# Optimization experiments

Measured on AMD Instinct MI355X. Metric: run time of the kernel, lower is better.

Reference implementation:

```python
import jax, jax.numpy as jnp
import numpy as np

MAX_ITER = 3  # matches init kwarg max_iter


def setup_inputs() -> dict:
    key = jax.random.key(0)
    k1, k2, k3, k4 = jax.random.split(key, 4)
    B, S = 4, 160
    return {
        "s_edge": jax.random.normal(k1, (B, S, S), dtype=jnp.float32),
        "s_sib": jax.random.normal(k2, (B, S, S, S), dtype=jnp.float32),
        "s_cop": jax.random.normal(k3, (B, S, S, S), dtype=jnp.float32),
        "s_grd": jax.random.normal(k4, (B, S, S, S), dtype=jnp.float32),
        "mask": jnp.ones((B, S, S), dtype=bool),
    }


def reference(s_edge, s_sib, s_cop, s_grd, mask):
    B, S, _ = mask.shape
    idx = jnp.arange(S)
    # Permute to the [head, mod, (sib), batch] layout used by the torch code.
    mask_p = jnp.transpose(mask, (2, 1, 0))              # [h, m, B]
    # 2nd-order mask: both (h,m) and (h,t) arcs valid, and t != h, t != m
    pair_ok = mask_p[:, None, :, :] & mask_p[:, :, None, :]   # [h, m, t, B]
    t_ok = (idx[:, None, None] != idx[None, None, :]) & (
        idx[None, :, None] != idx[None, None, :])             # [h, m, t]
    mask2o = (pair_ok & t_ok[..., None]).astype(s_edge.dtype)  # [h, m, t, B]

    se = jnp.transpose(s_edge, (2, 1, 0))                 # [h, m, B]
    ss = jnp.transpose(s_sib, (2, 1, 3, 0)) * mask2o      # [h, m, t, B]
    sc = jnp.transpose(s_cop, (2, 1, 3, 0)) * mask2o
    sg = jnp.transpose(s_grd, (2, 1, 3, 0)) * mask2o

    q = jnp.zeros((2, S, S, B), dtype=se.dtype)
    for _ in range(MAX_ITER):
        q1 = jax.nn.softmax(q, axis=0)[1]                 # [h, m, B]
        # f[h,m,b] = sum_t q1[h,t,b]*ss + q1[t,m,b]*sc + q1[m,t,b]*sg
        f = (jnp.einsum('htb,hmtb->hmb', q1, ss)
             + jnp.einsum('tmb,hmtb->hmb', q1, sc)
             + jnp.einsum('mtb,hmtb->hmb', q1, sg))
        q = jnp.stack([jnp.zeros_like(f), se + f])        # [2, h, m, B]

    logQ = jax.nn.log_softmax(jnp.transpose(q, (3, 2, 1, 0)), axis=-1)  # [B, m, h... -> B,S,S,2]
    return jnp.exp(logQ)
```

## Files before the change

### kernel.cpp

```cpp
#include <hip/hip_runtime.h>
#include <cmath>

typedef _Float16 hf;
typedef hf hf4 __attribute__((ext_vector_type(4)));

constexpr int S = 160;
constexpr int BATCH = 4;
constexpr int TPB = 256;

constexpr int KC = S / 4;
constexpr int LPR = 8;
constexpr int CPL = KC / LPR;
constexpr int RPB = TPB / LPR;
constexpr int NZ = S / RPB;

constexpr int FZSPLIT = 2;
constexpr int FROWS = S / FZSPLIT;
constexpr int FKC = S / 4;
constexpr int FLPR = 8;
constexpr int FCPL = FKC / FLPR;
constexpr int FRPP = TPB / FLPR;
constexpr int FPASSES = (FROWS + FRPP - 1) / FRPP;

__device__ __forceinline__ float sigmoidf_(float x) {
  return 1.0f / (1.0f + expf(-x));
}

__global__ void prep_wf(const int* __restrict__ mask, unsigned char* __restrict__ wf) {
  int i = blockIdx.x * blockDim.x + threadIdx.x;
  if (i >= BATCH * S * S) return;
  int t = i % S;
  int bh = i / S;
  int h = bh % S;
  int b = bh / S;
  wf[i] = (mask[(b * S + t) * S + h] != 0 && t != h) ? 1 : 0;
}

__global__ __launch_bounds__(TPB) void mfvi_first(
    const float* __restrict__ s_edge,
    const float* __restrict__ s_sib,
    const float* __restrict__ s_cop,
    const float* __restrict__ s_grd,
    const int* __restrict__ mask,
    const unsigned char* __restrict__ wf,
    hf* __restrict__ Aw, hf* __restrict__ Bw, hf* __restrict__ Cw,
    float* __restrict__ q1_out,
    float* __restrict__ q1t_out) {
  const int m = blockIdx.x;
  const int b = blockIdx.y;
  const int z = blockIdx.z;
  const int tid = threadIdx.x;

  __shared__ float sef[RPB];
  __shared__ float pmf[RPB];

  const size_t bm = (size_t)b * S + m;
  const int h0 = z * RPB;

  if (tid < RPB) {
    sef[tid] = s_edge[bm * S + h0 + tid];
    pmf[tid] = (mask[bm * S + h0 + tid] != 0) ? 1.0f : 0.0f;
  }
  __syncthreads();

  const int r = tid >> 3;
  const int j = tid & 7;
  const int h = h0 + r;

  const size_t rowf = (bm * S + h) * (size_t)S;
  const float4* SSr = (const float4*)(s_sib + rowf);
  const float4* CCr = (const float4*)(s_cop + rowf);
  const float4* GGr = (const float4*)(s_grd + rowf);
  const unsigned* WFr = (const unsigned*)(wf + ((size_t)b * S + h) * S);
  hf* Ar = Aw + rowf;
  hf* Br = Bw + rowf;
  hf* Cr = Cw + rowf;

  const int msel = m >> 2;
  const unsigned mclr = ~(255u << ((m & 3) * 8));
  const float pm = pmf[r];

  float4 sV[CPL], cV[CPL], gV[CPL];
  unsigned wV[CPL];
#pragma unroll
  for (int i = 0; i < CPL; ++i) {
    const int k = j + i * LPR;
    sV[i] = SSr[k];
    cV[i] = CCr[k];
    gV[i] = GGr[k];
    wV[i] = WFr[k];
  }

  float accA = 0.0f, accB = 0.0f, accC = 0.0f;
#pragma unroll
  for (int i = 0; i < CPL; ++i) {
    const int k = j + i * LPR;
    unsigned wu = wV[i];
    if (k == msel) wu &= mclr;
    const float w0 = (float)(wu & 255u) * pm;
    const float w1 = (float)((wu >> 8) & 255u) * pm;
    const float w2 = (float)((wu >> 16) & 255u) * pm;
    const float w3 = (float)(wu >> 24) * pm;
    const float a0 = w0 * sV[i].x, a1 = w1 * sV[i].y, a2 = w2 * sV[i].z, a3 = w3 * sV[i].w;
    const float b0 = w0 * cV[i].x, b1 = w1 * cV[i].y, b2 = w2 * cV[i].z, b3 = w3 * cV[i].w;
    const float e0 = w0 * gV[i].x, e1 = w1 * gV[i].y, e2 = w2 * gV[i].z, e3 = w3 * gV[i].w;
    accA += (a0 + a1) + (a2 + a3);
    accB += (b0 + b1) + (b2 + b3);
    accC += (e0 + e1) + (e2 + e3);
    hf4 A = {(hf)a0, (hf)a1, (hf)a2, (hf)a3};
    hf4 B = {(hf)b0, (hf)b1, (hf)b2, (hf)b3};
    hf4 C = {(hf)e0, (hf)e1, (hf)e2, (hf)e3};
    *(hf4*)(Ar + 4 * k) = A;
    *(hf4*)(Br + 4 * k) = B;
    *(hf4*)(Cr + 4 * k) = C;
  }
  float acc = accA + accB + accC;
  acc += __shfl_xor(acc, 1);
  acc += __shfl_xor(acc, 2);
  acc += __shfl_xor(acc, 4);
  if (j == 0) {
    const float qv = fmaf(0.5f, acc, sef[r]);
    const float sg1 = sigmoidf_(qv);
    q1_out[((size_t)b * S + h) * S + m] = sg1;
    q1t_out[bm * S + h] = sg1;
  }
}

template <bool LAST>
__global__ __launch_bounds__(TPB) void mfvi_next(
    const float* __restrict__ s_edge,
    const hf* __restrict__ Aw, const hf* __restrict__ Bw, const hf* __restrict__ Cw,
    const float* __restrict__ q1_in,
    const float* __restrict__ q1t_in,
    float* __restrict__ q1_out, float* __restrict__ q1t_out,
    float* __restrict__ outp) {
  const int m = blockIdx.x;
  const int b = blockIdx.y;
  const int z = blockIdx.z;
  const int tid = threadIdx.x;

  __shared__ __align__(16) float colm[S];
  __shared__ __align__(16) float rowm[S];
  __shared__ float sef[RPB];

  const size_t bm = (size_t)b * S + m;
  const int h0 = z * RPB;

  if (tid < S) {
    colm[tid] = q1t_in[bm * S + tid];
    rowm[tid] = q1_in[bm * S + tid];
    if (tid < RPB) sef[tid] = s_edge[bm * S + h0 + tid];
  }
  __syncthreads();

  const int r = tid >> 3;
  const int j = tid & 7;
  const int h = h0 + r;

  const size_t rowf = (bm * S + h) * (size_t)S;
  const hf* Ar = Aw + rowf;
  const hf* Br = Bw + rowf;
  const hf* Cr = Cw + rowf;
  const float4* Qr = (const float4*)(q1_in + ((size_t)b * S + h) * (size_t)S);

  hf4 aV[CPL], bV[CPL], cV[CPL];
  float4 qV[CPL];
#pragma unroll
  for (int i = 0; i < CPL; ++i) {
    const int k = j + i * LPR;
    aV[i] = *(const hf4*)(Ar + 4 * k);
    bV[i] = *(const hf4*)(Br + 4 * k);
    cV[i] = *(const hf4*)(Cr + 4 * k);
    qV[i] = Qr[k];
  }

  float accA = 0.0f, accB = 0.0f, accC = 0.0f;
#pragma unroll
  for (int i = 0; i < CPL; ++i) {
    const int k = j + i * LPR;
    const float4 cm = ((const float4*)colm)[k];
    const float4 rm = ((const float4*)rowm)[k];
    accA = fmaf(qV[i].x, (float)aV[i][0], accA);
    accA = fmaf(qV[i].y, (float)aV[i][1], accA);
    accA = fmaf(qV[i].z, (float)aV[i][2], accA);
    accA = fmaf(qV[i].w, (float)aV[i][3], accA);
    accB = fmaf(cm.x, (float)bV[i][0], accB);
    accB = fmaf(cm.y, (float)bV[i][1], accB);
    accB = fmaf(cm.z, (float)bV[i][2], accB);
    accB = fmaf(cm.w, (float)bV[i][3], accB);
    accC = fmaf(rm.x, (float)cV[i][0], accC);
    accC = fmaf(rm.y, (float)cV[i][1], accC);
    accC = fmaf(rm.z, (float)cV[i][2], accC);
    accC = fmaf(rm.w, (float)cV[i][3], accC);
  }
  float acc = accA + accB + accC;
  acc += __shfl_xor(acc, 1);
  acc += __shfl_xor(acc, 2);
  acc += __shfl_xor(acc, 4);
  if (j == 0) {
    const float qv = sef[r] + acc;
    if (!LAST) {
      const float sg1 = sigmoidf_(qv);
      q1_out[((size_t)b * S + h) * S + m] = sg1;
      q1t_out[bm * S + h] = sg1;
    } else {
      float2 o;
      o.x = sigmoidf_(-qv);
      o.y = sigmoidf_(qv);
      ((float2*)outp)[bm * S + h] = o;
    }
  }
}

template <bool FIRST, bool LAST>
__global__ __launch_bounds__(TPB, 4) void mfvi_iter(
    const float* __restrict__ s_edge, const float* __restrict__ s_sib,
    const float* __restrict__ s_cop, const float* __restrict__ s_grd,
    const int* __restrict__ mask, const unsigned char* __restrict__ wf,
    const float* __restrict__ q1_in, float* __restrict__ q1_out,
    float* __restrict__ outp) {
  const int m = blockIdx.x;
  const int b = blockIdx.y;
  const int z = blockIdx.z;
  const int tid = threadIdx.x;

  __shared__ __align__(16) float colm[S];
  __shared__ __align__(16) float rowm[S];
  __shared__ float sef[FROWS];
  __shared__ float pmf[FROWS];

  const float* G = q1_in + (size_t)b * S * S;
  const size_t bm = (size_t)b * S + m;
  const int h0 = z * FROWS;

  if (tid < S) {
    if (!FIRST) {
      colm[tid] = G[tid * S + m];
      rowm[tid] = G[m * S + tid];
    }
    if (tid < FROWS) {
      sef[tid] = s_edge[bm * S + h0 + tid];
      pmf[tid] = (mask[bm * S + h0 + tid] != 0) ? 1.0f : 0.0f;
    }
  }
  __syncthreads();

  const size_t blk = (bm * S + h0) * (size_t)S;
  const float4* SS = (const float4*)(s_sib + blk);
  const float4* CC = (const float4*)(s_cop + blk);
  const float4* GG = (const float4*)(s_grd + blk);
  const float4* QQ = (const float4*)(G + h0 * S);
  const unsigned* WF = (const unsigned*)(wf + ((size_t)b * S + h0) * S);
  const int msel = m >> 2;
  const unsigned mclr = ~(255u << ((m & 3) * 8));

  const int g = tid >> 3;
  const int j = tid & 7;

#pragma unroll
  for (int p = 0; p < FPASSES; ++p) {
    const int r = p * FRPP + g;
    if (r < FROWS) {
      const int rowbase = r * FKC;
      float acc = 0.0f;
#pragma unroll
      for (int i = 0; i < FCPL; ++i) {
        const int k = j + i * FLPR;
        const int c = rowbase + k;
        unsigned wu = WF[c];
        float4 s = SS[c];
        float4 cv = CC[c];
        float4 gv = GG[c];
        if (k == msel) wu &= mclr;
        float w0 = (float)(wu & 255u);
        float w1 = (float)((wu >> 8) & 255u);
        float w2 = (float)((wu >> 16) & 255u);
        float w3 = (float)(wu >> 24);
        if (FIRST) {
          float t0 = s.x + cv.x + gv.x;
          float t1 = s.y + cv.y + gv.y;
          float t2 = s.z + cv.z + gv.z;
          float t3 = s.w + cv.w + gv.w;
          acc = fmaf(w0, t0, fmaf(w1, t1, fmaf(w2, t2, fmaf(w3, t3, acc))));
        } else {
          float4 q = QQ[c];
          float4 cm = ((const float4*)colm)[k];
          float4 rm = ((const float4*)rowm)[k];
          float t0 = fmaf(q.x, s.x, fmaf(cm.x, cv.x, rm.x * gv.x));
          float t1 = fmaf(q.y, s.y, fmaf(cm.y, cv.y, rm.y * gv.y));
          float t2 = fmaf(q.z, s.z, fmaf(cm.z, cv.z, rm.z * gv.z));
          float t3 = fmaf(q.w, s.w, fmaf(cm.w, cv.w, rm.w * gv.w));
          acc = fmaf(w0, t0, fmaf(w1, t1, fmaf(w2, t2, fmaf(w3, t3, acc))));
        }
      }
      acc += __shfl_xor(acc, 1);
      acc += __shfl_xor(acc, 2);
      acc += __shfl_xor(acc, 4);
      if (j == 0) {
        const int h = h0 + r;
        const float qv = fmaf(pmf[r], FIRST ? 0.5f * acc : acc, sef[r]);
        if (!LAST) {
          q1_out[((size_t)b * S + h) * S + m] = sigmoidf_(qv);
        } else {
          float2 o;
          o.x = sigmoidf_(-qv);
          o.y = sigmoidf_(qv);
          ((float2*)outp)[bm * S + h] = o;
        }
      }
    }
  }
}

extern "C" void kernel_launch(void* const* d_in, const int* in_sizes, int n_in,
                              void* d_out, int out_size, void* d_ws, size_t ws_size,
                              hipStream_t stream) {
  const float* s_edge = (const float*)d_in[0];
  const float* s_sib = (const float*)d_in[1];
  const float* s_cop = (const float*)d_in[2];
  const float* s_grd = (const float*)d_in[3];
  const int* mask = (const int*)d_in[4];
  float* outp = (float*)d_out;

  const int qn = BATCH * S * S;
  const size_t NS3 = (size_t)BATCH * S * S * S;
  const size_t need = 3 * NS3 * sizeof(hf) + 4 * (size_t)qn * sizeof(float) + qn;

  if (ws_size >= need) {
    hf* Aw = (hf*)d_ws;
    hf* Bw = Aw + NS3;
    hf* Cw = Bw + NS3;
    float* q1B = (float*)(Cw + NS3);
    float* q1Bt = q1B + qn;
    float* q1A = q1Bt + qn;
    float* q1At = q1A + qn;
    unsigned char* wf = (unsigned char*)(q1At + qn);

    prep_wf<<<(qn + 255) / 256, 256, 0, stream>>>(mask, wf);

    dim3 grid(S, BATCH, NZ);
    mfvi_first<<<grid, TPB, 0, stream>>>(
        s_edge, s_sib, s_cop, s_grd, mask, wf, Aw, Bw, Cw, q1B, q1Bt);
    mfvi_next<false><<<grid, TPB, 0, stream>>>(
        s_edge, Aw, Bw, Cw, q1B, q1Bt, q1A, q1At, nullptr);
    mfvi_next<true><<<grid, TPB, 0, stream>>>(
        s_edge, Aw, Bw, Cw, q1A, q1At, nullptr, nullptr, outp);
  } else {
    float* q1A = (float*)d_ws;
    float* q1B = q1A + qn;
    unsigned char* wf = (unsigned char*)(q1B + qn);

    prep_wf<<<(qn + 255) / 256, 256, 0, stream>>>(mask, wf);

    dim3 grid(S, BATCH, FZSPLIT);
    mfvi_iter<true, false><<<grid, TPB, 0, stream>>>(
        s_edge, s_sib, s_cop, s_grd, mask, wf, q1A, q1B, nullptr);
    mfvi_iter<false, false><<<grid, TPB, 0, stream>>>(
        s_edge, s_sib, s_cop, s_grd, mask, wf, q1B, q1A, nullptr);
    mfvi_iter<false, true><<<grid, TPB, 0, stream>>>(
        s_edge, s_sib, s_cop, s_grd, mask, wf, q1A, nullptr, outp);
  }
}
```

Measured before the change: 263.2 us.

## Fuse all three MFVI iterations into one cooperative kernel with on-chip weight caching

Replaces the three separate iteration launches with a single cooperative kernel that uses grid-wide syncs between iterations. Each block keeps its masked sibling weights in LDS as fp16 and its coparent weights in registers. Only the grandparent weights are written to global memory and reloaded, which removes most of the fp16 tensor traffic in iterations two and three, along with the launch gaps. The cost is a large LDS footprint, register pressure and the need for all 1280 blocks to be co-resident. If the cooperative launch fails, it falls back to the old three-kernel path.

```diff
diff --git a/kernel.cpp b/kernel.cpp
--- a/kernel.cpp
+++ b/kernel.cpp
@@ -1,5 +1,8 @@
 #include <hip/hip_runtime.h>
+#include <hip/hip_cooperative_groups.h>
 #include <cmath>
+
+namespace cg = cooperative_groups;
 
 typedef _Float16 hf;
 typedef hf hf4 __attribute__((ext_vector_type(4)));
@@ -13,6 +16,10 @@
 constexpr int CPL = KC / LPR;
 constexpr int RPB = TPB / LPR;
 constexpr int NZ = S / RPB;
+
+constexpr int CR = 80;
+constexpr int CPASS = 3;
+constexpr int SIBP = 164;
 
 constexpr int FZSPLIT = 2;
 constexpr int FROWS = S / FZSPLIT;
@@ -36,16 +43,167 @@
   wf[i] = (mask[(b * S + t) * S + h] != 0 && t != h) ? 1 : 0;
 }
 
-__global__ __launch_bounds__(TPB) void mfvi_first(
+__global__ __launch_bounds__(TPB, 5) void mfvi_coop(
     const float* __restrict__ s_edge,
     const float* __restrict__ s_sib,
     const float* __restrict__ s_cop,
     const float* __restrict__ s_grd,
     const int* __restrict__ mask,
     const unsigned char* __restrict__ wf,
+    hf* __restrict__ Gw,
+    float* __restrict__ q1B, float* __restrict__ q1Bt,
+    float* __restrict__ q1A, float* __restrict__ q1At,
+    float* __restrict__ outp) {
+  cg::grid_group grid = cg::this_grid();
+  const int m = blockIdx.x;
+  const int b = blockIdx.y;
+  const int z = blockIdx.z;
+  const int tid = threadIdx.x;
+  const int r0 = tid >> 3;
+  const int j = tid & 7;
+  const size_t bm = (size_t)b * S + m;
+  const int h0 = z * CR;
+
+  __shared__ __align__(16) hf sibL[CR][SIBP];
+  __shared__ __align__(16) float colm[S];
+  __shared__ __align__(16) float rowm[S];
+  __shared__ float sef[CR];
+  __shared__ float pmf[CR];
+
+  if (tid < CR) {
+    sef[tid] = s_edge[bm * S + h0 + tid];
+    pmf[tid] = (mask[bm * S + h0 + tid] != 0) ? 1.0f : 0.0f;
+  }
+  __syncthreads();
+
+  const int msel = m >> 2;
+  const unsigned mclr = ~(255u << ((m & 3) * 8));
+
+  hf4 copReg[CPASS * CPL];
+
+#pragma unroll
+  for (int p = 0; p < CPASS; ++p) {
+    const int r = p * RPB + r0;
+    if (r < CR) {
+      const int h = h0 + r;
+      const float pm = pmf[r];
+      const size_t rowf = (bm * S + h) * (size_t)S;
+      const float4* SSr = (const float4*)(s_sib + rowf);
+      const float4* CCr = (const float4*)(s_cop + rowf);
+      const float4* GGr = (const float4*)(s_grd + rowf);
+      const unsigned* WFr = (const unsigned*)(wf + ((size_t)b * S + h) * S);
+      hf* Gr = Gw + rowf;
+      float acc = 0.0f;
+#pragma unroll
+      for (int i = 0; i < CPL; ++i) {
+        const int k = j + i * LPR;
+        unsigned wu = WFr[k];
+        float4 s = SSr[k];
+        float4 cv = CCr[k];
+        float4 gv = GGr[k];
+        if (k == msel) wu &= mclr;
+        const float w0 = (float)(wu & 255u) * pm;
+        const float w1 = (float)((wu >> 8) & 255u) * pm;
+        const float w2 = (float)((wu >> 16) & 255u) * pm;
+        const float w3 = (float)(wu >> 24) * pm;
+        const float a0 = w0 * s.x, a1 = w1 * s.y, a2 = w2 * s.z, a3 = w3 * s.w;
+        const float d0 = w0 * cv.x, d1 = w1 * cv.y, d2 = w2 * cv.z, d3 = w3 * cv.w;
+        const float e0 = w0 * gv.x, e1 = w1 * gv.y, e2 = w2 * gv.z, e3 = w3 * gv.w;
+        acc += ((a0 + d0 + e0) + (a1 + d1 + e1)) +
+               ((a2 + d2 + e2) + (a3 + d3 + e3));
+        hf4 A = {(hf)a0, (hf)a1, (hf)a2, (hf)a3};
+        hf4 D = {(hf)d0, (hf)d1, (hf)d2, (hf)d3};
+        hf4 E = {(hf)e0, (hf)e1, (hf)e2, (hf)e3};
+        *(hf4*)(&sibL[r][4 * k]) = A;
+        copReg[p * CPL + i] = D;
+        *(hf4*)(Gr + 4 * k) = E;
+      }
+      acc += __shfl_xor(acc, 1);
+      acc += __shfl_xor(acc, 2);
+      acc += __shfl_xor(acc, 4);
+      if (j == 0) {
+        const float qv = fmaf(0.5f, acc, sef[r]);
+        const float sg = sigmoidf_(qv);
+        q1B[((size_t)b * S + h) * S + m] = sg;
+        q1Bt[bm * S + h] = sg;
+      }
+    }
+  }
+  __threadfence();
+  grid.sync();
+
+#pragma unroll
+  for (int it = 0; it < 2; ++it) {
+    const bool last = (it == 1);
+    const float* qin = last ? q1A : q1B;
+    const float* qint = last ? q1At : q1Bt;
+    if (tid < S) {
+      colm[tid] = qint[bm * S + tid];
+      rowm[tid] = qin[bm * S + tid];
+    }
+    __syncthreads();
+#pragma unroll
+    for (int p = 0; p < CPASS; ++p) {
+      const int r = p * RPB + r0;
+      if (r < CR) {
+        const int h = h0 + r;
+        const float4* Qr = (const float4*)(qin + ((size_t)b * S + h) * (size_t)S);
+        const hf* Gr = Gw + (bm * S + h) * (size_t)S;
+        float accA = 0.0f, accB = 0.0f, accC = 0.0f;
+#pragma unroll
+        for (int i = 0; i < CPL; ++i) {
+          const int k = j + i * LPR;
+          float4 q = Qr[k];
+          float4 cm = ((const float4*)colm)[k];
+          float4 rm = ((const float4*)rowm)[k];
+          hf4 A = *(const hf4*)(&sibL[r][4 * k]);
+          hf4 D = copReg[p * CPL + i];
+          hf4 E = *(const hf4*)(Gr + 4 * k);
+          accA = fmaf(q.x, (float)A[0], accA);
+          accA = fmaf(q.y, (float)A[1], accA);
+          accA = fmaf(q.z, (float)A[2], accA);
+          accA = fmaf(q.w, (float)A[3], accA);
+          accB = fmaf(cm.x, (float)D[0], accB);
+          accB = fmaf(cm.y, (float)D[1], accB);
+          accB = fmaf(cm.z, (float)D[2], accB);
+          accB = fmaf(cm.w, (float)D[3], accB);
+          accC = fmaf(rm.x, (float)E[0], accC);
+          accC = fmaf(rm.y, (float)E[1], accC);
+          accC = fmaf(rm.z, (float)E[2], accC);
+          accC = fmaf(rm.w, (float)E[3], accC);
+        }
+        float acc = accA + accB + accC;
+        acc += __shfl_xor(acc, 1);
+        acc += __shfl_xor(acc, 2);
+        acc += __shfl_xor(acc, 4);
+        if (j == 0) {
+          const float qv = sef[r] + acc;
+          if (!last) {
+            const float sg = sigmoidf_(qv);
+            q1A[((size_t)b * S + h) * S + m] = sg;
+            q1At[bm * S + h] = sg;
+          } else {
+            float2 o;
+            o.x = sigmoidf_(-qv);
+            o.y = sigmoidf_(qv);
+            ((float2*)outp)[bm * S + h] = o;
+          }
+        }
+      }
+    }
+    if (!last) {
+      __threadfence();
+      grid.sync();
+    }
+  }
+}
+
+__global__ __launch_bounds__(TPB) void mfvi_first(
+    const float* __restrict__ s_edge, const float* __restrict__ s_sib,
+    const float* __restrict__ s_cop, const float* __restrict__ s_grd,
+    const int* __restrict__ mask, const unsigned char* __restrict__ wf,
     hf* __restrict__ Aw, hf* __restrict__ Bw, hf* __restrict__ Cw,
-    float* __restrict__ q1_out,
-    float* __restrict__ q1t_out) {
+    float* __restrict__ q1_out, float* __restrict__ q1t_out) {
   const int m = blockIdx.x;
   const int b = blockIdx.y;
   const int z = blockIdx.z;
@@ -80,30 +238,22 @@
   const unsigned mclr = ~(255u << ((m & 3) * 8));
   const float pm = pmf[r];
 
-  float4 sV[CPL], cV[CPL], gV[CPL];
-  unsigned wV[CPL];
+  float accA = 0.0f, accB = 0.0f, accC = 0.0f;
 #pragma unroll
   for (int i = 0; i < CPL; ++i) {
     const int k = j + i * LPR;
-    sV[i] = SSr[k];
-    cV[i] = CCr[k];
-    gV[i] = GGr[k];
-    wV[i] = WFr[k];
-  }
-
-  float accA = 0.0f, accB = 0.0f, accC = 0.0f;
-#pragma unroll
-  for (int i = 0; i < CPL; ++i) {
-    const int k = j + i * LPR;
-    unsigned wu = wV[i];
+    unsigned wu = WFr[k];
+    float4 s = SSr[k];
+    float4 cv = CCr[k];
+    float4 gv = GGr[k];
     if (k == msel) wu &= mclr;
     const float w0 = (float)(wu & 255u) * pm;
     const float w1 = (float)((wu >> 8) & 255u) * pm;
     const float w2 = (float)((wu >> 16) & 255u) * pm;
     const float w3 = (float)(wu >> 24) * pm;
-    const float a0 = w0 * sV[i].x, a1 = w1 * sV[i].y, a2 = w2 * sV[i].z, a3 = w3 * sV[i].w;
-    const float b0 = w0 * cV[i].x, b1 = w1 * cV[i].y, b2 = w2 * cV[i].z, b3 = w3 * cV[i].w;
-    const float e0 = w0 * gV[i].x, e1 = w1 * gV[i].y, e2 = w2 * gV[i].z, e3 = w3 * gV[i].w;
+    const float a0 = w0 * s.x, a1 = w1 * s.y, a2 = w2 * s.z, a3 = w3 * s.w;
+    const float b0 = w0 * cv.x, b1 = w1 * cv.y, b2 = w2 * cv.z, b3 = w3 * cv.w;
+    const float e0 = w0 * gv.x, e1 = w1 * gv.y, e2 = w2 * gv.z, e3 = w3 * gv.w;
     accA += (a0 + a1) + (a2 + a3);
     accB += (b0 + b1) + (b2 + b3);
     accC += (e0 + e1) + (e2 + e3);
@@ -130,8 +280,7 @@
 __global__ __launch_bounds__(TPB) void mfvi_next(
     const float* __restrict__ s_edge,
     const hf* __restrict__ Aw, const hf* __restrict__ Bw, const hf* __restrict__ Cw,
-    const float* __restrict__ q1_in,
-    const float* __restrict__ q1t_in,
+    const float* __restrict__ q1_in, const float* __restrict__ q1t_in,
     float* __restrict__ q1_out, float* __restrict__ q1t_out,
     float* __restrict__ outp) {
   const int m = blockIdx.x;
@@ -163,35 +312,28 @@
   const hf* Cr = Cw + rowf;
   const float4* Qr = (const float4*)(q1_in + ((size_t)b * S + h) * (size_t)S);
 
-  hf4 aV[CPL], bV[CPL], cV[CPL];
-  float4 qV[CPL];
+  float accA = 0.0f, accB = 0.0f, accC = 0.0f;
 #pragma unroll
   for (int i = 0; i < CPL; ++i) {
     const int k = j + i * LPR;
-    aV[i] = *(const hf4*)(Ar + 4 * k);
-    bV[i] = *(const hf4*)(Br + 4 * k);
-    cV[i] = *(const hf4*)(Cr + 4 * k);
-    qV[i] = Qr[k];
-  }
-
-  float accA = 0.0f, accB = 0.0f, accC = 0.0f;
-#pragma unroll
-  for (int i = 0; i < CPL; ++i) {
-    const int k = j + i * LPR;
+    hf4 A = *(const hf4*)(Ar + 4 * k);
+    hf4 B = *(const hf4*)(Br + 4 * k);
+    hf4 C = *(const hf4*)(Cr + 4 * k);
+    float4 q = Qr[k];
     const float4 cm = ((const float4*)colm)[k];
     const float4 rm = ((const float4*)rowm)[k];
-    accA = fmaf(qV[i].x, (float)aV[i][0], accA);
-    accA = fmaf(qV[i].y, (float)aV[i][1], accA);
-    accA = fmaf(qV[i].z, (float)aV[i][2], accA);
-    accA = fmaf(qV[i].w, (float)aV[i][3], accA);
-    accB = fmaf(cm.x, (float)bV[i][0], accB);
-    accB = fmaf(cm.y, (float)bV[i][1], accB);
-    accB = fmaf(cm.z, (float)bV[i][2], accB);
-    accB = fmaf(cm.w, (float)bV[i][3], accB);
-    accC = fmaf(rm.x, (float)cV[i][0], accC);
-    accC = fmaf(rm.y, (float)cV[i][1], accC);
-    accC = fmaf(rm.z, (float)cV[i][2], accC);
-    accC = fmaf(rm.w, (float)cV[i][3], accC);
+    accA = fmaf(q.x, (float)A[0], accA);
+    accA = fmaf(q.y, (float)A[1], accA);
+    accA = fmaf(q.z, (float)A[2], accA);
+    accA = fmaf(q.w, (float)A[3], accA);
+    accB = fmaf(cm.x, (float)B[0], accB);
+    accB = fmaf(cm.y, (float)B[1], accB);
+    accB = fmaf(cm.z, (float)B[2], accB);
+    accB = fmaf(cm.w, (float)B[3], accB);
+    accC = fmaf(rm.x, (float)C[0], accC);
+    accC = fmaf(rm.y, (float)C[1], accC);
+    accC = fmaf(rm.z, (float)C[2], accC);
+    accC = fmaf(rm.w, (float)C[3], accC);
   }
   float acc = accA + accB + accC;
   acc += __shfl_xor(acc, 1);
@@ -338,13 +480,24 @@
 
     prep_wf<<<(qn + 255) / 256, 256, 0, stream>>>(mask, wf);
 
-    dim3 grid(S, BATCH, NZ);
-    mfvi_first<<<grid, TPB, 0, stream>>>(
-        s_edge, s_sib, s_cop, s_grd, mask, wf, Aw, Bw, Cw, q1B, q1Bt);
-    mfvi_next<false><<<grid, TPB, 0, stream>>>(
-        s_edge, Aw, Bw, Cw, q1B, q1Bt, q1A, q1At, nullptr);
-    mfvi_next<true><<<grid, TPB, 0, stream>>>(
-        s_edge, Aw, Bw, Cw, q1A, q1At, nullptr, nullptr, outp);
+    void* args[] = {
+        (void*)&s_edge, (void*)&s_sib, (void*)&s_cop, (void*)&s_grd,
+        (void*)&mask,   (void*)&wf,    (void*)&Cw,
+        (void*)&q1B,    (void*)&q1Bt,  (void*)&q1A,   (void*)&q1At,
+        (void*)&outp};
+    hipError_t e = hipLaunchCooperativeKernel(
+        (const void*)mfvi_coop, dim3(S, BATCH, 2), dim3(TPB, 1, 1), args, 0,
+        stream);
+    if (e != hipSuccess) {
+      (void)hipGetLastError();
+      dim3 grid(S, BATCH, NZ);
+      mfvi_first<<<grid, TPB, 0, stream>>>(
+          s_edge, s_sib, s_cop, s_grd, mask, wf, Aw, Bw, Cw, q1B, q1Bt);
+      mfvi_next<false><<<grid, TPB, 0, stream>>>(
+          s_edge, Aw, Bw, Cw, q1B, q1Bt, q1A, q1At, nullptr);
+      mfvi_next<true><<<grid, TPB, 0, stream>>>(
+          s_edge, Aw, Bw, Cw, q1A, q1At, nullptr, nullptr, outp);
+    }
   } else {
     float* q1A = (float*)d_ws;
     float* q1B = q1A + qn;
```

After: 873.6 us. 232% more time.
